# Performance work log

Hardware: AMD Instinct MI355X
Metric: run time of the kernel (lower is better)

The kernel has to match this reference:

```python
import jax, jax.numpy as jnp
import numpy as np

N_CONVS = 16
K = 9                 # 3x3 patch -> in_features of KANLinear
GRID_SIZE = 5
SPLINE_ORDER = 3
N_BASES = GRID_SIZE + SPLINE_ORDER  # 8
# extended grid: (grid_size + 2*order + 1) = 12 knots on [-1,1] with h=2/grid_size
_H = 2.0 / GRID_SIZE
GRID = (jnp.arange(-SPLINE_ORDER, GRID_SIZE + SPLINE_ORDER + 1, dtype=jnp.float32) * _H - 1.0)


def b_splines(x):
    """x: [N, K] -> bases: [N, K, N_BASES] (Cox-de Boor recursion, efficient-kan)."""
    g = GRID
    xe = x[..., None]  # [N, K, 1]
    bases = ((xe >= g[:-1]) & (xe < g[1:])).astype(x.dtype)  # degree 0: [N,K,11]
    for k in range(1, SPLINE_ORDER + 1):
        left = (xe - g[: -(k + 1)]) / (g[k:-1] - g[: -(k + 1)]) * bases[..., :-1]
        right = (g[k + 1:] - xe) / (g[k + 1:] - g[1:-k]) * bases[..., 1:]
        bases = left + right
    return bases  # [N, K, 8]


def setup_inputs() -> dict:
    key = jax.random.key(0)
    ks = jax.random.split(key, 6)
    B, C, Hh, Ww = 8, 1, 384, 384
    x = jax.random.normal(ks[0], (B, C, Hh, Ww), dtype=jnp.float32)
    # per-conv KANLinear(9 -> 1) parameters
    base_weight = jax.random.normal(ks[1], (N_CONVS, K), dtype=jnp.float32) * (1.0 / np.sqrt(K))
    spline_weight = jax.random.normal(ks[2], (N_CONVS, K, N_BASES), dtype=jnp.float32) * 0.1
    spline_scaler = jax.random.normal(ks[3], (N_CONVS, K), dtype=jnp.float32) * (1.0 / np.sqrt(K))
    # restore Conv2d(n_convs, 1, 3, padding=1)
    restore_w = jax.random.normal(ks[4], (1, N_CONVS, 3, 3), dtype=jnp.float32) * (1.0 / np.sqrt(N_CONVS * 9))
    restore_b = jax.random.normal(ks[5], (1,), dtype=jnp.float32) * 0.01
    return {"x": x, "base_weight": base_weight, "spline_weight": spline_weight,
            "spline_scaler": spline_scaler, "restore_w": restore_w, "restore_b": restore_b}


def reference(x, base_weight, spline_weight, spline_scaler, restore_w, restore_b):
    B, C, Hh, Ww = x.shape  # C == 1
    # im2col: 3x3 patches with padding 1 -> [B, 9, H, W]
    patches = jax.lax.conv_general_dilated_patches(
        x, filter_shape=(3, 3), window_strides=(1, 1), padding=((1, 1), (1, 1)))
    p = patches.transpose(0, 2, 3, 1).reshape(-1, K)  # [N, 9], N = B*H*W
    # KANLinear: base branch (SiLU) + spline branch, for all n_convs at once
    silu_p = p * jax.nn.sigmoid(p)
    base_out = jnp.einsum('nk,ck->nc', silu_p, base_weight)           # [N, n_convs]
    bs = b_splines(p)                                                  # [N, 9, 8]
    scaled_sw = spline_weight * spline_scaler[..., None]               # [C,9,8]
    spline_out = jnp.einsum('nkb,ckb->nc', bs, scaled_sw)              # [N, n_convs]
    y = (base_out + spline_out).reshape(B, Hh, Ww, N_CONVS).transpose(0, 3, 1, 2)
    # restore conv 3x3, pad 1
    out = jax.lax.conv_general_dilated(
        y, restore_w, window_strides=(1, 1), padding=((1, 1), (1, 1)),
        dimension_numbers=('NCHW', 'OIHW', 'NCHW'))
    return out + restore_b[None, :, None, None]
```

## Files before the change

kernel.cpp:

```cpp
#include <hip/hip_runtime.h>


#define HW 384
#define NIMG 8
#define NPX (NIMG * HW * HW)

#define TW 64
#define TH 16
#define FROWS (TH + 4)
#define FCOLS 68
#define NGRP 17
#define FPOS (FROWS * FCOLS)

#define NBORD 1532
#define WS_WC 0
#define WS_CORR 1024

__device__ __forceinline__ void kan_feats(float x, float f[9]) {
  float sg = __builtin_amdgcn_rcpf(1.0f + __expf(-x));
  f[0] = x * sg;
  float u = (x + 2.2f) * 2.5f;
  float fj = floorf(u);
  int j = (int)fj;
  float t = u - fj;
  float omt = 1.0f - t;
  float t2 = t * t, t3 = t2 * t;
  float w0 = (1.0f / 6.0f) * omt * omt * omt;
  float w3 = (1.0f / 6.0f) * t3;
  float w1 = fmaf(0.5f, t3, fmaf(-1.0f, t2, 2.0f / 3.0f));
  float w2 = fmaf(-0.5f, t3, fmaf(0.5f, t2, fmaf(0.5f, t, 1.0f / 6.0f)));
#pragma unroll
  for (int i = 0; i < 8; ++i) {
    int d = i + 3 - j;
    float v = (d < 2) ? ((d == 0) ? w0 : w1) : ((d == 2) ? w2 : w3);
    f[1 + i] = ((unsigned)d <= 3u) ? v : 0.0f;
  }
}

__global__ void kan_prep(const float* __restrict__ bw, const float* __restrict__ sw,
                         const float* __restrict__ ss, const float* __restrict__ rw,
                         const float* __restrict__ x, float* __restrict__ ws) {
  __shared__ float l_bw[144], l_ss[144], l_rw[144], l_sw[1152], l_h[729];
  const int tid = threadIdx.x;
  for (int i = tid; i < 144; i += 256) { l_bw[i] = bw[i]; l_ss[i] = ss[i]; l_rw[i] = rw[i]; }
  for (int i = tid; i < 1152; i += 256) l_sw[i] = sw[i];
  __syncthreads();
  for (int i = tid; i < 729; i += 256) {
    int f = i % 9, dk = i / 9, d = dk / 9, k = dk % 9;
    float acc = 0.f;
#pragma unroll
    for (int c = 0; c < 16; ++c) {
      float wfv = (f == 0) ? l_bw[c * 9 + k] : l_sw[(c * 9 + k) * 8 + (f - 1)] * l_ss[c * 9 + k];
      acc = fmaf(l_rw[c * 9 + d], wfv, acc);
    }
    l_h[i] = acc;
  }
  __syncthreads();

  if (blockIdx.x == 0) {
    if (tid < 225) {
      int f = tid / 25, e = tid % 25, ey = e / 5 - 2, ex = e % 5 - 2;
      float acc = 0.f;
#pragma unroll
      for (int d = 0; d < 9; ++d) {
        int dy = d / 3 - 1, dx = d % 3 - 1;
        int ky = ey - dy, kx = ex - dx;
        if (ky < -1 || ky > 1 || kx < -1 || kx > 1) continue;
        int k = (ky + 1) * 3 + (kx + 1);
        acc += l_h[(d * 9 + k) * 9 + f];
      }
      ws[WS_WC + tid] = acc;
    }
  } else {
    int gid = (blockIdx.x - 1) * 256 + tid;
    if (gid < NIMG * NBORD) {
      int img = gid / NBORD, rem = gid % NBORD;
      int pr, pc;
      if (rem < 384)       { pr = 0;              pc = rem; }
      else if (rem < 768)  { pr = 383;            pc = rem - 384; }
      else if (rem < 1150) { pr = rem - 768 + 1;  pc = 0; }
      else                 { pr = rem - 1150 + 1; pc = 383; }
      const float* xim = x + img * HW * HW;
      float corrv = 0.f;
#pragma unroll
      for (int dy = -1; dy <= 1; ++dy)
#pragma unroll
        for (int dx = -1; dx <= 1; ++dx) {
          int qr = pr + dy, qc = pc + dx;
          if (qr >= 0 && qr < HW && qc >= 0 && qc < HW) continue;
          const int d = (dy + 1) * 3 + (dx + 1);
#pragma unroll
          for (int ky = -1; ky <= 1; ++ky)
#pragma unroll
            for (int kx = -1; kx <= 1; ++kx) {
              int sr = qr + ky, sc = qc + kx;
              float v = (sr >= 0 && sr < HW && sc >= 0 && sc < HW) ? xim[sr * HW + sc] : 0.0f;
              float fv[9];
              kan_feats(v, fv);
              const int k = (ky + 1) * 3 + (kx + 1);
              float t = 0.f;
#pragma unroll
              for (int ft = 0; ft < 9; ++ft) t = fmaf(l_h[(d * 9 + k) * 9 + ft], fv[ft], t);
              corrv += t;
            }
        }
      ws[WS_CORR + gid] = corrv;
    }
  }
}

__launch_bounds__(256)
__global__ void kan_main(const float* __restrict__ x, const float* __restrict__ ws,
                         const float* __restrict__ rbp, float* __restrict__ out) {
  __shared__ __align__(16) float Fp[9][FPOS];
  const float* Wc = ws + WS_WC;
  const float* corr = ws + WS_CORR;
  const int tx0 = blockIdx.x * TW, ty0 = blockIdx.y * TH, img = blockIdx.z;
  const float* xim = x + img * HW * HW;
  const int tid = threadIdx.y * 16 + threadIdx.x;

#pragma unroll
  for (int it = 0; it < 6; ++it) {
    int id = it * 256 + tid;
    if (id < FPOS) {
      int r = id / FCOLS, cl = id - r * FCOLS;
      int row = ty0 + r - 2, col = tx0 + cl - 2;
      float v = (row >= 0 && row < HW && col >= 0 && col < HW) ? xim[row * HW + col] : 0.0f;
      float f[9];
      kan_feats(v, f);
      int g = (cl >> 2) + ((r >> 1) & 3);
      if (g >= NGRP) g -= NGRP;
      const int pos = r * FCOLS + (g << 2) + (cl & 3);
#pragma unroll
      for (int ft = 0; ft < 9; ++ft) Fp[ft][pos] = f[ft];
    }
  }
  __syncthreads();

  const int txi = threadIdx.x, tyi = threadIdx.y;
  int adr[5][2];
#pragma unroll
  for (int ey = 0; ey < 5; ++ey) {
    const int rr = tyi + ey;
    const int s = (rr >> 1) & 3;
    int ga = txi + s;     if (ga >= NGRP) ga -= NGRP;
    int gb = txi + 1 + s; if (gb >= NGRP) gb -= NGRP;
    adr[ey][0] = rr * FCOLS + (ga << 2);
    adr[ey][1] = rr * FCOLS + (gb << 2);
  }

  float acc[4] = {0.f, 0.f, 0.f, 0.f};
#pragma unroll
  for (int f = 0; f < 9; ++f) {
#pragma unroll
    for (int ey = 0; ey < 5; ++ey) {
      const float4 wa = *(const float4*)&Fp[f][adr[ey][0]];
      const float4 wb = *(const float4*)&Fp[f][adr[ey][1]];
      const float w[8] = {wa.x, wa.y, wa.z, wa.w, wb.x, wb.y, wb.z, wb.w};
#pragma unroll
      for (int ex = 0; ex < 5; ++ex) {
        const float wt = Wc[f * 25 + ey * 5 + ex];
#pragma unroll
        for (int c = 0; c < 4; ++c)
          acc[c] = fmaf(wt, w[c + ex], acc[c]);
      }
    }
  }

  const float rb = rbp[0];
  const bool edgeblk = (tx0 == 0) | (tx0 == HW - TW) | (ty0 == 0) | (ty0 == HW - TH);
  float* oim = out + img * HW * HW;
  const int row = ty0 + tyi;
  const int col0 = tx0 + 4 * txi;
  float v[4];
#pragma unroll
  for (int c = 0; c < 4; ++c) v[c] = acc[c] + rb;
  if (edgeblk) {
#pragma unroll
    for (int c = 0; c < 4; ++c) {
      const int col = col0 + c;
      int bidx = -1;
      if (row == 0)            bidx = col;
      else if (row == HW - 1)  bidx = 384 + col;
      else if (col == 0)       bidx = 768 + row - 1;
      else if (col == HW - 1)  bidx = 1150 + row - 1;
      if (bidx >= 0) v[c] -= corr[img * NBORD + bidx];
    }
  }
  *(float4*)&oim[row * HW + col0] = make_float4(v[0], v[1], v[2], v[3]);
}

__global__ void kan_direct(const float* __restrict__ x, const float* __restrict__ bw,
                           const float* __restrict__ sw, const float* __restrict__ ss,
                           const float* __restrict__ rw, const float* __restrict__ rbp,
                           float* __restrict__ out) {
  int idx = blockIdx.x * 256 + threadIdx.x;
  if (idx >= NPX) return;
  int img = idx / (HW * HW), rem = idx % (HW * HW);
  int pr = rem / HW, pc = rem % HW;
  const float* xim = x + img * HW * HW;
  float acc = rbp[0];
  for (int dy = -1; dy <= 1; ++dy)
    for (int dx = -1; dx <= 1; ++dx) {
      int qr = pr + dy, qc = pc + dx;
      if (qr < 0 || qr >= HW || qc < 0 || qc >= HW) continue;
      const int d = (dy + 1) * 3 + (dx + 1);
      for (int ky = -1; ky <= 1; ++ky)
        for (int kx = -1; kx <= 1; ++kx) {
          int sr = qr + ky, sc = qc + kx;
          float v = (sr >= 0 && sr < HW && sc >= 0 && sc < HW) ? xim[sr * HW + sc] : 0.0f;
          float f[9];
          kan_feats(v, f);
          const int k = (ky + 1) * 3 + (kx + 1);
          for (int c = 0; c < 16; ++c) {
            float spl = 0.f;
            for (int b = 0; b < 8; ++b) spl = fmaf(sw[(c * 9 + k) * 8 + b], f[1 + b], spl);
            acc = fmaf(rw[c * 9 + d], fmaf(bw[c * 9 + k], f[0], ss[c * 9 + k] * spl), acc);
          }
        }
    }
  out[idx] = acc;
}

extern "C" void kernel_launch(void* const* d_in, const int* in_sizes, int n_in,
                              void* d_out, int out_size, void* d_ws, size_t ws_size,
                              hipStream_t stream) {
  const float* x  = (const float*)d_in[0];
  const float* bw = (const float*)d_in[1];
  const float* sw = (const float*)d_in[2];
  const float* ss = (const float*)d_in[3];
  const float* rw = (const float*)d_in[4];
  const float* rb = (const float*)d_in[5];
  float* out = (float*)d_out;

  const size_t ws_need = (size_t)(WS_CORR + NIMG * NBORD) * sizeof(float);
  if (ws_size >= ws_need && d_ws != nullptr) {
    float* ws = (float*)d_ws;
    kan_prep<<<1 + (NIMG * NBORD + 255) / 256, 256, 0, stream>>>(bw, sw, ss, rw, x, ws);
    dim3 grid(HW / TW, HW / TH, NIMG), blk(16, 16);
    kan_main<<<grid, blk, 0, stream>>>(x, ws, rb, out);
  } else {
    kan_direct<<<(NPX + 255) / 256, 256, 0, stream>>>(x, bw, sw, ss, rw, rb, out);
  }
}
```

Baseline: 110.5 us.

## Store spline basis features as fp16 in LDS with a widened swizzle stride

The eight B-spline basis features are now stored in shared memory as half precision, while the SiLU base feature stays fp32 in its own array. The row stride grows to 72 with 18 swizzle groups so the half-width layout stays aligned and conflict-reduced. This roughly halves LDS footprint and LDS read traffic per tile, which may allow more resident blocks. In exchange it adds fp16-to-fp32 conversions in the inner loop and rounds the basis weights, which costs some accuracy.

New measurement: 103.7 us. 1.06x faster.

```diff
diff --git a/kernel.cpp b/kernel.cpp
--- a/kernel.cpp
+++ b/kernel.cpp
@@ -9,12 +9,15 @@
 #define TH 16
 #define FROWS (TH + 4)
 #define FCOLS 68
-#define NGRP 17
+#define FSTR 72
+#define NGRP 18
 #define FPOS (FROWS * FCOLS)
 
 #define NBORD 1532
 #define WS_WC 0
 #define WS_CORR 1024
+
+typedef _Float16 half4v __attribute__((ext_vector_type(4)));
 
 __device__ __forceinline__ void kan_feats(float x, float f[9]) {
   float sg = __builtin_amdgcn_rcpf(1.0f + __expf(-x));
@@ -112,7 +115,8 @@
 __launch_bounds__(256)
 __global__ void kan_main(const float* __restrict__ x, const float* __restrict__ ws,
                          const float* __restrict__ rbp, float* __restrict__ out) {
-  __shared__ __align__(16) float Fp[9][FPOS];
+  __shared__ __align__(16) float F0[FROWS * FSTR];
+  __shared__ __align__(16) _Float16 Fs[8][FROWS * FSTR];
   const float* Wc = ws + WS_WC;
   const float* corr = ws + WS_CORR;
   const int tx0 = blockIdx.x * TW, ty0 = blockIdx.y * TH, img = blockIdx.z;
@@ -130,9 +134,10 @@
       kan_feats(v, f);
       int g = (cl >> 2) + ((r >> 1) & 3);
       if (g >= NGRP) g -= NGRP;
-      const int pos = r * FCOLS + (g << 2) + (cl & 3);
-#pragma unroll
-      for (int ft = 0; ft < 9; ++ft) Fp[ft][pos] = f[ft];
+      const int pos = r * FSTR + (g << 2) + (cl & 3);
+      F0[pos] = f[0];
+#pragma unroll
+      for (int ft = 0; ft < 8; ++ft) Fs[ft][pos] = (_Float16)f[1 + ft];
     }
   }
   __syncthreads();
@@ -145,21 +150,35 @@
     const int s = (rr >> 1) & 3;
     int ga = txi + s;     if (ga >= NGRP) ga -= NGRP;
     int gb = txi + 1 + s; if (gb >= NGRP) gb -= NGRP;
-    adr[ey][0] = rr * FCOLS + (ga << 2);
-    adr[ey][1] = rr * FCOLS + (gb << 2);
+    adr[ey][0] = rr * FSTR + (ga << 2);
+    adr[ey][1] = rr * FSTR + (gb << 2);
   }
 
   float acc[4] = {0.f, 0.f, 0.f, 0.f};
 #pragma unroll
-  for (int f = 0; f < 9; ++f) {
+  for (int ey = 0; ey < 5; ++ey) {
+    const float4 wa = *(const float4*)&F0[adr[ey][0]];
+    const float4 wb = *(const float4*)&F0[adr[ey][1]];
+    const float w[8] = {wa.x, wa.y, wa.z, wa.w, wb.x, wb.y, wb.z, wb.w};
+#pragma unroll
+    for (int ex = 0; ex < 5; ++ex) {
+      const float wt = Wc[ey * 5 + ex];
+#pragma unroll
+      for (int c = 0; c < 4; ++c)
+        acc[c] = fmaf(wt, w[c + ex], acc[c]);
+    }
+  }
+#pragma unroll
+  for (int f = 0; f < 8; ++f) {
 #pragma unroll
     for (int ey = 0; ey < 5; ++ey) {
-      const float4 wa = *(const float4*)&Fp[f][adr[ey][0]];
-      const float4 wb = *(const float4*)&Fp[f][adr[ey][1]];
-      const float w[8] = {wa.x, wa.y, wa.z, wa.w, wb.x, wb.y, wb.z, wb.w};
+      const half4v ha = *(const half4v*)&Fs[f][adr[ey][0]];
+      const half4v hb = *(const half4v*)&Fs[f][adr[ey][1]];
+      const float w[8] = {(float)ha.x, (float)ha.y, (float)ha.z, (float)ha.w,
+                          (float)hb.x, (float)hb.y, (float)hb.z, (float)hb.w};
 #pragma unroll
       for (int ex = 0; ex < 5; ++ex) {
-        const float wt = Wc[f * 25 + ey * 5 + ex];
+        const float wt = Wc[(1 + f) * 25 + ey * 5 + ex];
 #pragma unroll
         for (int c = 0; c < 4; ++c)
           acc[c] = fmaf(wt, w[c + ex], acc[c]);
```
